# Kernel optimization log

Hardware: AMD Instinct MI355X
Metric: run time of the kernel (lower is better)

Reference implementation:

```python
import jax, jax.numpy as jnp
import numpy as np

IN_FEATURES = 1024
NUM_EXPERTS = 64
TOP_K = 2


def setup_inputs() -> dict:
    key = jax.random.key(0)
    kx, kw, kb = jax.random.split(key, 3)
    x = jax.random.normal(kx, (8, 4096, IN_FEATURES), dtype=jnp.float32)
    # nn.Linear init scale ~ 1/sqrt(in_features)
    bound = 1.0 / np.sqrt(IN_FEATURES)
    W = jax.random.uniform(kw, (NUM_EXPERTS, IN_FEATURES), dtype=jnp.float32, minval=-bound, maxval=bound)
    b = jax.random.uniform(kb, (NUM_EXPERTS,), dtype=jnp.float32, minval=-bound, maxval=bound)
    return {"x": x, "W": W, "b": b}


def reference(x, W, b):
    # logits: [B, S, E]
    logits = jnp.einsum("bsd,ed->bse", x, W) + b
    gates = jax.nn.softmax(logits, axis=-1)
    top_k_gates, top_k_indices = jax.lax.top_k(gates, TOP_K)
    return top_k_gates, top_k_indices
```

## Files before the change

### kernel.cpp

```cpp
#include <hip/hip_runtime.h>

#define D 1024
#define E 64
#define TPB 256
#define TOKS 16
#define KSW 8

typedef __attribute__((ext_vector_type(8))) short bf16x8;
typedef __attribute__((ext_vector_type(8))) unsigned short u16x8;
typedef __attribute__((ext_vector_type(4))) float f32x4;
typedef __attribute__((ext_vector_type(4))) unsigned int u32x4;

__device__ __forceinline__ unsigned short bf16_rne(float f) {
    unsigned u = __builtin_bit_cast(unsigned, f);
    u += 0x7fffu + ((u >> 16) & 1u);
    return (unsigned short)(u >> 16);
}
__device__ __forceinline__ float bf16_to_f(unsigned short h) {
    unsigned u = ((unsigned)h) << 16;
    return __builtin_bit_cast(float, u);
}
__device__ __forceinline__ unsigned cvt_pk_bf16(float a, float b) {
    unsigned r;
    asm("v_cvt_pk_bf16_f32 %0, %1, %2" : "=v"(r) : "v"(a), "v"(b));
    return r;
}
__device__ __forceinline__ float lo_val(unsigned p) {
    return __builtin_bit_cast(float, p << 16);
}
__device__ __forceinline__ float hi_val(unsigned p) {
    return __builtin_bit_cast(float, p & 0xffff0000u);
}

struct Afrag { f32x4 u, v; };
struct Bfrag { bf16x8 f0, f1, f2, f3, f4, f5, f6, f7; };

__device__ __forceinline__ void split8_rne(f32x4 a, f32x4 b, bf16x8& hv, bf16x8& lv) {
    unsigned h0 = cvt_pk_bf16(a[0], a[1]);
    unsigned h1 = cvt_pk_bf16(a[2], a[3]);
    unsigned h2 = cvt_pk_bf16(b[0], b[1]);
    unsigned h3 = cvt_pk_bf16(b[2], b[3]);
    unsigned l0 = cvt_pk_bf16(a[0] - lo_val(h0), a[1] - hi_val(h0));
    unsigned l1 = cvt_pk_bf16(a[2] - lo_val(h1), a[3] - hi_val(h1));
    unsigned l2 = cvt_pk_bf16(b[0] - lo_val(h2), b[1] - hi_val(h2));
    unsigned l3 = cvt_pk_bf16(b[2] - lo_val(h3), b[3] - hi_val(h3));
    hv = __builtin_bit_cast(bf16x8, (u32x4){h0, h1, h2, h3});
    lv = __builtin_bit_cast(bf16x8, (u32x4){l0, l1, l2, l3});
}

__global__ __launch_bounds__(TPB) void router_prep(
        const float* __restrict__ W, unsigned short* __restrict__ Ws) {
    int t = blockIdx.x * TPB + threadIdx.x;
    int lane = t & 63;
    int nt = (t >> 6) & 3;
    int ks = t >> 8;
    int n = lane & 15, q = lane >> 4;
    const float* src = W + (size_t)(nt * 16 + n) * D + ks * 32 + q * 8;
    u16x8 hv, lv;
#pragma unroll
    for (int j = 0; j < 8; ++j) {
        float v = src[j];
        unsigned short h = bf16_rne(v);
        hv[j] = h;
        lv[j] = bf16_rne(v - bf16_to_f(h));
    }
    size_t base = ((size_t)(ks * 8 + nt * 2) * 64 + lane) * 8;
    *(u16x8*)(Ws + base)          = hv;
    *(u16x8*)(Ws + base + 64 * 8) = lv;
}

__global__ __launch_bounds__(TPB, 4) void router_main(
        const float* __restrict__ x, const unsigned short* __restrict__ Ws,
        const float* __restrict__ bias, float* __restrict__ out, int T) {
    __shared__ __align__(16) float part[4][TOKS][E];
    __shared__ float ls[TOKS][E + 1];
    __shared__ float sbias[E];

    const int tid  = threadIdx.x;
    const int lane = tid & 63;
    const int wid  = tid >> 6;
    const int n    = lane & 15;
    const int q    = lane >> 4;
    const int t0   = blockIdx.x * TOKS;
    const int kb   = wid * KSW;

    if (tid < E) sbias[tid] = bias[tid];

    const float* arow = x + (size_t)(t0 + n) * D + q * 8;
    const bf16x8* bptr = (const bf16x8*)Ws + lane;

    f32x4 c0 = {0.f, 0.f, 0.f, 0.f}, c1 = c0, c2 = c0, c3 = c0;
    bf16x8 ah, al;
    Afrag A0, A1;
    Bfrag Bt;

#define LOADA(A_, ks_) do {                                   \
        A_.u = *(const f32x4*)(arow + (ks_) * 32);            \
        A_.v = *(const f32x4*)(arow + (ks_) * 32 + 4);        \
    } while (0)

#define LOADB(ks_) do {                                       \
        const bf16x8* _p = bptr + (size_t)(ks_) * 512;        \
        Bt.f0 = _p[0];   Bt.f1 = _p[64];  Bt.f2 = _p[128];    \
        Bt.f3 = _p[192]; Bt.f4 = _p[256]; Bt.f5 = _p[320];    \
        Bt.f6 = _p[384]; Bt.f7 = _p[448];                     \
    } while (0)

#define MFMA __builtin_amdgcn_mfma_f32_16x16x32_bf16
#define COMP() do {                                           \
        c0 = MFMA(ah, Bt.f0, c0, 0, 0, 0);                    \
        c0 = MFMA(al, Bt.f0, c0, 0, 0, 0);                    \
        c0 = MFMA(ah, Bt.f1, c0, 0, 0, 0);                    \
        c1 = MFMA(ah, Bt.f2, c1, 0, 0, 0);                    \
        c1 = MFMA(al, Bt.f2, c1, 0, 0, 0);                    \
        c1 = MFMA(ah, Bt.f3, c1, 0, 0, 0);                    \
        c2 = MFMA(ah, Bt.f4, c2, 0, 0, 0);                    \
        c2 = MFMA(al, Bt.f4, c2, 0, 0, 0);                    \
        c2 = MFMA(ah, Bt.f5, c2, 0, 0, 0);                    \
        c3 = MFMA(ah, Bt.f6, c3, 0, 0, 0);                    \
        c3 = MFMA(al, Bt.f6, c3, 0, 0, 0);                    \
        c3 = MFMA(ah, Bt.f7, c3, 0, 0, 0);                    \
    } while (0)

    LOADA(A0, kb + 0);
    LOADA(A1, kb + 1);

#pragma unroll
    for (int kk = 0; kk < KSW; kk += 2) {
        {
            LOADB(kb + kk);
            split8_rne(A0.u, A0.v, ah, al);
            const int kr = (kk + 2 < KSW) ? kk + 2 : KSW - 1;
            LOADA(A0, kb + kr);
            COMP();
        }
        {
            LOADB(kb + kk + 1);
            split8_rne(A1.u, A1.v, ah, al);
            const int kr = (kk + 3 < KSW) ? kk + 3 : KSW - 1;
            LOADA(A1, kb + kr);
            COMP();
        }
    }

    {
        const int row = q * 4;
#define STORE_P(c_, nt_) do {                                 \
            int col = (nt_) * 16 + n;                         \
            part[wid][row + 0][col] = c_[0];                  \
            part[wid][row + 1][col] = c_[1];                  \
            part[wid][row + 2][col] = c_[2];                  \
            part[wid][row + 3][col] = c_[3];                  \
        } while (0)
        STORE_P(c0, 0); STORE_P(c1, 1); STORE_P(c2, 2); STORE_P(c3, 3);
#undef STORE_P
    }
    __syncthreads();

#pragma unroll
    for (int j = 0; j < 4; ++j) {
        int idx = tid + j * TPB;
        int tok = idx >> 6, e = idx & 63;
        float s = ((part[0][tok][e] + part[1][tok][e]) + part[2][tok][e])
                  + part[3][tok][e];
        ls[tok][e] = s + sbias[e];
    }
    __syncthreads();

    if (tid < TOKS) {
        float m1 = -3.4e38f, m2 = -3.4e38f;
        int i1 = 0, i2 = 0;
        for (int e = 0; e < E; ++e) {
            float v = ls[tid][e];
            if (v > m1) { m2 = m1; i2 = i1; m1 = v; i1 = e; }
            else if (v > m2) { m2 = v; i2 = e; }
        }
        float Z = 0.f;
        for (int e = 0; e < E; ++e) Z += __expf(ls[tid][e] - m1);
        float inv = 1.f / Z;
        int gt = t0 + tid;
        out[(size_t)gt * 2]     = inv;
        out[(size_t)gt * 2 + 1] = __expf(m2 - m1) * inv;
        float* oi = out + (size_t)T * 2;
        oi[(size_t)gt * 2]     = (float)i1;
        oi[(size_t)gt * 2 + 1] = (float)i2;
    }
}

extern "C" void kernel_launch(void* const* d_in, const int* in_sizes, int n_in,
                              void* d_out, int out_size, void* d_ws, size_t ws_size,
                              hipStream_t stream) {
    const float* x = (const float*)d_in[0];
    const float* W = (const float*)d_in[1];
    const float* b = (const float*)d_in[2];
    float* out = (float*)d_out;
    unsigned short* Ws = (unsigned short*)d_ws;
    int T = in_sizes[0] / D;
    hipLaunchKernelGGL(router_prep, dim3(32), dim3(TPB), 0, stream, W, Ws);
    hipLaunchKernelGGL(router_main, dim3(T / TOKS), dim3(TPB), 0, stream,
                       x, Ws, b, out, T);
}
```

Baseline: 227.6 us.

## Stage bf16-split x tile in LDS and use eight waves per block

```diff
diff --git a/kernel.cpp b/kernel.cpp
--- a/kernel.cpp
+++ b/kernel.cpp
@@ -2,9 +2,14 @@
 
 #define D 1024
 #define E 64
-#define TPB 256
+#define TPB 512
 #define TOKS 16
-#define KSW 8
+#define NW 8
+#define KSW 4
+
+#define SPR 129
+#define ROWB (SPR * 16)
+#define TILEB (16 * ROWB)
 
 typedef __attribute__((ext_vector_type(8))) short bf16x8;
 typedef __attribute__((ext_vector_type(8))) unsigned short u16x8;
@@ -32,7 +37,6 @@
     return __builtin_bit_cast(float, p & 0xffff0000u);
 }
 
-struct Afrag { f32x4 u, v; };
 struct Bfrag { bf16x8 f0, f1, f2, f3, f4, f5, f6, f7; };
 
 __device__ __forceinline__ void split8_rne(f32x4 a, f32x4 b, bf16x8& hv, bf16x8& lv) {
@@ -48,9 +52,9 @@
     lv = __builtin_bit_cast(bf16x8, (u32x4){l0, l1, l2, l3});
 }
 
-__global__ __launch_bounds__(TPB) void router_prep(
+__global__ __launch_bounds__(256) void router_prep(
         const float* __restrict__ W, unsigned short* __restrict__ Ws) {
-    int t = blockIdx.x * TPB + threadIdx.x;
+    int t = blockIdx.x * 256 + threadIdx.x;
     int lane = t & 63;
     int nt = (t >> 6) & 3;
     int ks = t >> 8;
@@ -72,9 +76,10 @@
 __global__ __launch_bounds__(TPB, 4) void router_main(
         const float* __restrict__ x, const unsigned short* __restrict__ Ws,
         const float* __restrict__ bias, float* __restrict__ out, int T) {
-    __shared__ __align__(16) float part[4][TOKS][E];
-    __shared__ float ls[TOKS][E + 1];
-    __shared__ float sbias[E];
+    __shared__ __align__(16) union SM {
+        unsigned char tile[2 * TILEB];
+        struct { float part[NW][TOKS][E]; float ls[TOKS][E + 1]; } r;
+    } sm;
 
     const int tid  = threadIdx.x;
     const int lane = tid & 63;
@@ -82,22 +87,29 @@
     const int n    = lane & 15;
     const int q    = lane >> 4;
     const int t0   = blockIdx.x * TOKS;
-    const int kb   = wid * KSW;
-
-    if (tid < E) sbias[tid] = bias[tid];
-
-    const float* arow = x + (size_t)(t0 + n) * D + q * 8;
+
+    {
+        const float* xt = x + (size_t)t0 * D;
+#pragma unroll
+        for (int i = 0; i < 4; ++i) {
+            int j = tid + i * TPB;
+            int row = j >> 7, col8 = j & 127;
+            const float* g = xt + (size_t)row * D + col8 * 8;
+            f32x4 a = *(const f32x4*)g;
+            f32x4 b = *(const f32x4*)(g + 4);
+            bf16x8 hv, lv;
+            split8_rne(a, b, hv, lv);
+            char* base = (char*)sm.tile + row * ROWB + col8 * 16;
+            *(bf16x8*)base           = hv;
+            *(bf16x8*)(base + TILEB) = lv;
+        }
+    }
+    __syncthreads();
+
+    f32x4 c0 = {0.f, 0.f, 0.f, 0.f}, c1 = c0, c2 = c0, c3 = c0;
+    Bfrag Bt;
     const bf16x8* bptr = (const bf16x8*)Ws + lane;
-
-    f32x4 c0 = {0.f, 0.f, 0.f, 0.f}, c1 = c0, c2 = c0, c3 = c0;
-    bf16x8 ah, al;
-    Afrag A0, A1;
-    Bfrag Bt;
-
-#define LOADA(A_, ks_) do {                                   \
-        A_.u = *(const f32x4*)(arow + (ks_) * 32);            \
-        A_.v = *(const f32x4*)(arow + (ks_) * 32 + 4);        \
-    } while (0)
+    const char* arow_h = (const char*)sm.tile + n * ROWB + q * 16;
 
 #define LOADB(ks_) do {                                       \
         const bf16x8* _p = bptr + (size_t)(ks_) * 512;        \
@@ -107,50 +119,41 @@
     } while (0)
 
 #define MFMA __builtin_amdgcn_mfma_f32_16x16x32_bf16
-#define COMP() do {                                           \
-        c0 = MFMA(ah, Bt.f0, c0, 0, 0, 0);                    \
-        c0 = MFMA(al, Bt.f0, c0, 0, 0, 0);                    \
-        c0 = MFMA(ah, Bt.f1, c0, 0, 0, 0);                    \
-        c1 = MFMA(ah, Bt.f2, c1, 0, 0, 0);                    \
-        c1 = MFMA(al, Bt.f2, c1, 0, 0, 0);                    \
-        c1 = MFMA(ah, Bt.f3, c1, 0, 0, 0);                    \
-        c2 = MFMA(ah, Bt.f4, c2, 0, 0, 0);                    \
-        c2 = MFMA(al, Bt.f4, c2, 0, 0, 0);                    \
-        c2 = MFMA(ah, Bt.f5, c2, 0, 0, 0);                    \
-        c3 = MFMA(ah, Bt.f6, c3, 0, 0, 0);                    \
-        c3 = MFMA(al, Bt.f6, c3, 0, 0, 0);                    \
-        c3 = MFMA(ah, Bt.f7, c3, 0, 0, 0);                    \
+#define COMP(ah_, al_) do {                                   \
+        c0 = MFMA(ah_, Bt.f0, c0, 0, 0, 0);                   \
+        c0 = MFMA(al_, Bt.f0, c0, 0, 0, 0);                   \
+        c0 = MFMA(ah_, Bt.f1, c0, 0, 0, 0);                   \
+        c1 = MFMA(ah_, Bt.f2, c1, 0, 0, 0);                   \
+        c1 = MFMA(al_, Bt.f2, c1, 0, 0, 0);                   \
+        c1 = MFMA(ah_, Bt.f3, c1, 0, 0, 0);                   \
+        c2 = MFMA(ah_, Bt.f4, c2, 0, 0, 0);                   \
+        c2 = MFMA(al_, Bt.f4, c2, 0, 0, 0);                   \
+        c2 = MFMA(ah_, Bt.f5, c2, 0, 0, 0);                   \
+        c3 = MFMA(ah_, Bt.f6, c3, 0, 0, 0);                   \
+        c3 = MFMA(al_, Bt.f6, c3, 0, 0, 0);                   \
+        c3 = MFMA(ah_, Bt.f7, c3, 0, 0, 0);                   \
     } while (0)
 
-    LOADA(A0, kb + 0);
-    LOADA(A1, kb + 1);
-
-#pragma unroll
-    for (int kk = 0; kk < KSW; kk += 2) {
-        {
-            LOADB(kb + kk);
-            split8_rne(A0.u, A0.v, ah, al);
-            const int kr = (kk + 2 < KSW) ? kk + 2 : KSW - 1;
-            LOADA(A0, kb + kr);
-            COMP();
-        }
-        {
-            LOADB(kb + kk + 1);
-            split8_rne(A1.u, A1.v, ah, al);
-            const int kr = (kk + 3 < KSW) ? kk + 3 : KSW - 1;
-            LOADA(A1, kb + kr);
-            COMP();
-        }
-    }
+#pragma unroll
+    for (int kk = 0; kk < KSW; ++kk) {
+        const int ks = (wid << 2) + kk;
+        LOADB(ks);
+        const char* p = arow_h + ks * 64;
+        bf16x8 ah = *(const bf16x8*)p;
+        bf16x8 al = *(const bf16x8*)(p + TILEB);
+        COMP(ah, al);
+    }
+
+    __syncthreads();
 
     {
         const int row = q * 4;
 #define STORE_P(c_, nt_) do {                                 \
             int col = (nt_) * 16 + n;                         \
-            part[wid][row + 0][col] = c_[0];                  \
-            part[wid][row + 1][col] = c_[1];                  \
-            part[wid][row + 2][col] = c_[2];                  \
-            part[wid][row + 3][col] = c_[3];                  \
+            sm.r.part[wid][row + 0][col] = c_[0];             \
+            sm.r.part[wid][row + 1][col] = c_[1];             \
+            sm.r.part[wid][row + 2][col] = c_[2];             \
+            sm.r.part[wid][row + 3][col] = c_[3];             \
         } while (0)
         STORE_P(c0, 0); STORE_P(c1, 1); STORE_P(c2, 2); STORE_P(c3, 3);
 #undef STORE_P
@@ -158,12 +161,18 @@
     __syncthreads();
 
 #pragma unroll
-    for (int j = 0; j < 4; ++j) {
-        int idx = tid + j * TPB;
+    for (int i = 0; i < 2; ++i) {
+        int idx = tid + i * TPB;
         int tok = idx >> 6, e = idx & 63;
-        float s = ((part[0][tok][e] + part[1][tok][e]) + part[2][tok][e])
-                  + part[3][tok][e];
-        ls[tok][e] = s + sbias[e];
+        float s = sm.r.part[0][tok][e];
+        s += sm.r.part[1][tok][e];
+        s += sm.r.part[2][tok][e];
+        s += sm.r.part[3][tok][e];
+        s += sm.r.part[4][tok][e];
+        s += sm.r.part[5][tok][e];
+        s += sm.r.part[6][tok][e];
+        s += sm.r.part[7][tok][e];
+        sm.r.ls[tok][e] = s + bias[e];
     }
     __syncthreads();
 
@@ -171,12 +180,12 @@
         float m1 = -3.4e38f, m2 = -3.4e38f;
         int i1 = 0, i2 = 0;
         for (int e = 0; e < E; ++e) {
-            float v = ls[tid][e];
+            float v = sm.r.ls[tid][e];
             if (v > m1) { m2 = m1; i2 = i1; m1 = v; i1 = e; }
             else if (v > m2) { m2 = v; i2 = e; }
         }
         float Z = 0.f;
-        for (int e = 0; e < E; ++e) Z += __expf(ls[tid][e] - m1);
+        for (int e = 0; e < E; ++e) Z += __expf(sm.r.ls[tid][e] - m1);
         float inv = 1.f / Z;
         int gt = t0 + tid;
         out[(size_t)gt * 2]     = inv;
@@ -196,7 +205,7 @@
     float* out = (float*)d_out;
     unsigned short* Ws = (unsigned short*)d_ws;
     int T = in_sizes[0] / D;
-    hipLaunchKernelGGL(router_prep, dim3(32), dim3(TPB), 0, stream, W, Ws);
+    hipLaunchKernelGGL(router_prep, dim3(32), dim3(256), 0, stream, W, Ws);
     hipLaunchKernelGGL(router_main, dim3(T / TOKS), dim3(TPB), 0, stream,
                        x, Ws, b, out, T);
 }
```

Measured after the change: 227.8 us. No clear change (+0.1%).
